# Kernel tuning notes

Measured on AMD Instinct MI355X. Metric: run time of the kernel, lower is better.

Reference implementation:

```python
import jax, jax.numpy as jnp
import numpy as np


def setup_inputs() -> dict:
    key = jax.random.key(0)
    ks = jax.random.split(key, 13)
    B, T, F = 4096, 512, 64
    P, M = 64, 64  # price / metrics embedding dims
    TD, ED = 1, 8  # target_dim, explanatory_dim
    s = 0.05
    return {
        "input_seq": jax.random.normal(ks[0], (B, T, F), jnp.float32),
        "m_Wih": jax.random.normal(ks[1], (M, F + P), jnp.float32) * s,
        "m_Whh": jax.random.normal(ks[2], (M, M), jnp.float32) * s,
        "m_bih": jax.random.normal(ks[3], (M,), jnp.float32) * s,
        "m_bhh": jax.random.normal(ks[4], (M,), jnp.float32) * s,
        "p_Wih": jax.random.normal(ks[5], (P, F + M), jnp.float32) * s,
        "p_Whh": jax.random.normal(ks[6], (P, P), jnp.float32) * s,
        "p_bih": jax.random.normal(ks[7], (P,), jnp.float32) * s,
        "p_bhh": jax.random.normal(ks[8], (P,), jnp.float32) * s,
        "price_lin_W": jax.random.normal(ks[9], (TD, P), jnp.float32) * s,
        "price_lin_b": jax.random.normal(ks[10], (TD,), jnp.float32) * s,
        "metrics_lin_W": jax.random.normal(ks[11], (ED, M), jnp.float32) * s,
        "metrics_lin_b": jax.random.normal(ks[12], (ED,), jnp.float32) * s,
    }


def reference(input_seq, m_Wih, m_Whh, m_bih, m_bhh,
              p_Wih, p_Whh, p_bih, p_bhh,
              price_lin_W, price_lin_b, metrics_lin_W, metrics_lin_b):
    B = input_seq.shape[0]
    P = p_Whh.shape[0]
    M = m_Whh.shape[0]
    p0 = jnp.zeros((B, P), input_seq.dtype)
    m0 = jnp.zeros((B, M), input_seq.dtype)

    def step(carry, x_t):  # x_t: [B, F]
        p, m = carry
        # metrics cell: input = cat(x_t, price_embedding)
        m = jnp.tanh(jnp.concatenate([x_t, p], axis=1) @ m_Wih.T + m_bih
                     + m @ m_Whh.T + m_bhh)
        # price cell: input = cat(x_t, metrics_embedding)
        p = jnp.tanh(jnp.concatenate([x_t, m], axis=1) @ p_Wih.T + p_bih
                     + p @ p_Whh.T + p_bhh)
        return (p, m), None

    (p, m), _ = jax.lax.scan(step, (p0, m0), jnp.swapaxes(input_seq, 0, 1))
    # dropout in eval mode = identity
    price_pred = p @ price_lin_W.T + price_lin_b
    metrics_pred = m @ metrics_lin_W.T + metrics_lin_b
    return (price_pred, metrics_pred)
```

## Files before the change

kernel.cpp:

```cpp
#include <hip/hip_runtime.h>

typedef short bf16x8 __attribute__((ext_vector_type(8)));
typedef float f32x4 __attribute__((ext_vector_type(4)));
typedef int   int4v  __attribute__((ext_vector_type(4)));

#define MFMA16(a, b, c) __builtin_amdgcn_mfma_f32_16x16x32_bf16((a), (b), (c), 0, 0, 0)

static constexpr int T_LEN = 512;
static constexpr int F_DIM = 64;
static constexpr int NB    = 8;
static constexpr float C1  = 2.885390081777927f;

__device__ __forceinline__ unsigned short brne(float f) {
  unsigned u = __float_as_uint(f);
  return (unsigned short)((u + 0x7fffu + ((u >> 16) & 1u)) >> 16);
}

__device__ __forceinline__ int cvtpk(float lo, float hi) {
  int r;
  asm("v_cvt_pk_bf16_f32 %0, %1, %2" : "=v"(r) : "v"(lo), "v"(hi));
  return r;
}

__device__ __forceinline__ bf16x8 cvt8(const float4 &a, const float4 &b) {
  int4v d = {cvtpk(a.x, a.y), cvtpk(a.z, a.w), cvtpk(b.x, b.y), cvtpk(b.z, b.w)};
  union { int4v i; bf16x8 h; } u;
  u.i = d;
  return u.h;
}

__device__ __forceinline__ void swap32(float &a, float &b) {
  auto r = __builtin_amdgcn_permlane32_swap(__float_as_int(a), __float_as_int(b),
                                            false, false);
  a = __int_as_float(r[0]);
  b = __int_as_float(r[1]);
}

__device__ __forceinline__ float xor1(float v) {
  return __int_as_float(__builtin_amdgcn_mov_dpp(__float_as_int(v), 0xB1, 0xF, 0xF, true));
}

__device__ __forceinline__ float tanh_fold(float s, float c2) {
  float e  = __builtin_amdgcn_exp2f(__builtin_fmaf(s, C1, c2));
  float rc = __builtin_amdgcn_rcpf(e + 1.0f);
  return __builtin_fmaf(-2.0f, rc, 1.0f);
}

__device__ __forceinline__ void bar() {
  asm volatile("s_waitcnt lgkmcnt(0)" ::: "memory");
  __builtin_amdgcn_s_barrier();
  __builtin_amdgcn_sched_barrier(0);
}

template<int PAR, bool FIN>
__device__ __forceinline__ void epilogue(
    const f32x4 &a0, const f32x4 &a1, float c2,
    unsigned short (*buf)[72], float (*fin)[68],
    int wofs, bool evn, int rowA, int j)
{
  float z0 = a0[0] + a1[0];
  float z1 = a0[1] + a1[1];
  float z2 = a0[2] + a1[2];
  float z3 = a0[3] + a1[3];
  swap32(z0, z2);
  swap32(z1, z3);
  float sA = (PAR == 0) ? z0 : z2;
  float sB = (PAR == 0) ? z1 : z3;
  float tA = tanh_fold(sA, c2);
  float tB = tanh_fold(sB, c2);
  float nA = xor1(tA);
  float nB = xor1(tB);
  if (evn) {
    unsigned short *p = &buf[0][0];
    *(unsigned *)(p + wofs)      = (unsigned)cvtpk(tA, nA);
    *(unsigned *)(p + wofs + 72) = (unsigned)cvtpk(tB, nB);
  }
  if (FIN) {
    fin[rowA][j]     = tA;
    fin[rowA + 1][j] = tB;
  }
}

template<int PAR, bool FIN>
__device__ __forceinline__ void step_cells(
    int arow, int g8, int j, int wofs, bool evn, int rowA,
    const bf16x8 &x0, const bf16x8 &x1,
    const bf16x8 (&Bm)[6], const bf16x8 (&Bp)[6],
    float c2m, float c2p, const f32x4 &Z,
    unsigned short (*sm_c)[72], unsigned short (*sm_p)[72],
    unsigned short (*sp_c)[72], unsigned short (*sp_p)[72],
    float (*mfin)[68], float (*pfin)[68])
{
  bf16x8 p0 = *(const bf16x8 *)&sp_p[arow][g8];
  bf16x8 p1 = *(const bf16x8 *)&sp_p[arow][32 + g8];
  bf16x8 m0 = *(const bf16x8 *)&sm_p[arow][g8];
  bf16x8 m1 = *(const bf16x8 *)&sm_p[arow][32 + g8];

  f32x4 a0 = MFMA16(x0, Bm[0], Z);
  f32x4 a1 = MFMA16(x1, Bm[1], Z);
  a0 = MFMA16(p0, Bm[2], a0);
  a1 = MFMA16(p1, Bm[3], a1);
  a0 = MFMA16(m0, Bm[4], a0);
  a1 = MFMA16(m1, Bm[5], a1);
  f32x4 b0 = MFMA16(x0, Bp[0], Z);
  f32x4 b1 = MFMA16(x1, Bp[1], Z);
  b0 = MFMA16(p0, Bp[4], b0);
  b1 = MFMA16(p1, Bp[5], b1);
  epilogue<PAR, FIN>(a0, a1, c2m, sm_c, mfin, wofs, evn, rowA, j);
  bar();
  {
    bf16x8 n0 = *(const bf16x8 *)&sm_c[arow][g8];
    bf16x8 n1 = *(const bf16x8 *)&sm_c[arow][32 + g8];
    b0 = MFMA16(n0, Bp[2], b0);
    b1 = MFMA16(n1, Bp[3], b1);
    epilogue<PAR, FIN>(b0, b1, c2p, sp_c, pfin, wofs, evn, rowA, j);
  }
  bar();
}

__global__ __launch_bounds__(256, 2)
void mr_rnn_kernel(const float *__restrict__ x,
                   const float *__restrict__ mWih, const float *__restrict__ mWhh,
                   const float *__restrict__ mbih, const float *__restrict__ mbhh,
                   const float *__restrict__ pWih, const float *__restrict__ pWhh,
                   const float *__restrict__ pbih, const float *__restrict__ pbhh,
                   const float *__restrict__ plW,  const float *__restrict__ plb,
                   const float *__restrict__ mlW,  const float *__restrict__ mlb,
                   float *__restrict__ out, int B)
{
  __shared__ __align__(16) unsigned short sm[2][NB][72], sp[2][NB][72];
  __shared__ __align__(16) float s_mfin[NB][68], s_pfin[NB][68];

  const int tid  = threadIdx.x;
  const int lane = tid & 63;
  const int q    = tid >> 6;
  const int l15  = lane & 15;
  const int arow = l15 & (NB - 1);
  const int half = l15 >> 3;
  const int g    = lane >> 4;
  const int j    = q * 16 + l15;
  const int b0   = blockIdx.x * NB;
  const int g8   = g * 8;
  const int rowA = ((lane & 16) >> 2) | ((lane >> 5) << 1);
  const bool evn = (l15 & 1) == 0;
  const int wofs = rowA * 72 + (j & ~1);

  bf16x8 Bm[6], Bp[6];
#pragma unroll
  for (int kt = 0; kt < 6; ++kt) {
    const int k0 = kt * 32 + g8;
#pragma unroll
    for (int i = 0; i < 8; ++i) {
      const int k = k0 + i;
      float wm = (k < 128) ? mWih[j * 128 + k] : mWhh[j * 64 + (k - 128)];
      float wp = (k < 128) ? pWih[j * 128 + k] : pWhh[j * 64 + (k - 128)];
      Bm[kt][i] = (short)brne(wm);
      Bp[kt][i] = (short)brne(wp);
    }
  }
  const float c2m = C1 * (mbih[j] + mbhh[j]);
  const float c2p = C1 * (pbih[j] + pbhh[j]);
  const f32x4 Z = {0.f, 0.f, 0.f, 0.f};

  for (int idx = tid; idx < NB * 72; idx += 256) {
    const int bb = idx / 72, kk = idx % 72;
    sm[1][bb][kk] = 0;
    sp[1][bb][kk] = 0;
  }

  const float *pxl = x + ((size_t)(b0 + arow) * T_LEN + half) * F_DIM + g8;
  float4 A0 = *(const float4 *)(pxl);
  float4 A1 = *(const float4 *)(pxl + 4);
  float4 A2 = *(const float4 *)(pxl + 32);
  float4 A3 = *(const float4 *)(pxl + 36);
  bf16x8 x0 = cvt8(A0, A1);
  bf16x8 x1 = cvt8(A2, A3);
  __syncthreads();

#pragma unroll 1
  for (int t = 0; t < T_LEN - 2; t += 2) {
    pxl += 2 * F_DIM;
    A0 = *(const float4 *)(pxl);
    A1 = *(const float4 *)(pxl + 4);
    A2 = *(const float4 *)(pxl + 32);
    A3 = *(const float4 *)(pxl + 36);
    step_cells<0, false>(arow, g8, j, wofs, evn, rowA, x0, x1, Bm, Bp, c2m, c2p, Z,
                         sm[0], sm[1], sp[0], sp[1], s_mfin, s_pfin);
    step_cells<1, false>(arow, g8, j, wofs, evn, rowA, x0, x1, Bm, Bp, c2m, c2p, Z,
                         sm[1], sm[0], sp[1], sp[0], s_mfin, s_pfin);
    x0 = cvt8(A0, A1);
    x1 = cvt8(A2, A3);
  }
  step_cells<0, false>(arow, g8, j, wofs, evn, rowA, x0, x1, Bm, Bp, c2m, c2p, Z,
                       sm[0], sm[1], sp[0], sp[1], s_mfin, s_pfin);
  step_cells<1, true>(arow, g8, j, wofs, evn, rowA, x0, x1, Bm, Bp, c2m, c2p, Z,
                      sm[1], sm[0], sp[1], sp[0], s_mfin, s_pfin);

  if (tid < NB) {
    const int b = tid;
    float acc = plb[0];
#pragma unroll 1
    for (int k = 0; k < 64; ++k) acc += s_pfin[b][k] * plW[k];
    out[b0 + b] = acc;
  } else if (tid < NB + NB * 8) {
    const int r = tid - NB;
    const int b = r >> 3, e = r & 7;
    float acc = mlb[e];
#pragma unroll 1
    for (int k = 0; k < 64; ++k) acc += s_mfin[b][k] * mlW[e * 64 + k];
    out[(size_t)B + (size_t)(b0 + b) * 8 + e] = acc;
  }
}

extern "C" void kernel_launch(void* const* d_in, const int* in_sizes, int n_in,
                              void* d_out, int out_size, void* d_ws, size_t ws_size,
                              hipStream_t stream) {
  (void)n_in; (void)out_size; (void)d_ws; (void)ws_size;
  const float* x    = (const float*)d_in[0];
  const float* mWih = (const float*)d_in[1];
  const float* mWhh = (const float*)d_in[2];
  const float* mbih = (const float*)d_in[3];
  const float* mbhh = (const float*)d_in[4];
  const float* pWih = (const float*)d_in[5];
  const float* pWhh = (const float*)d_in[6];
  const float* pbih = (const float*)d_in[7];
  const float* pbhh = (const float*)d_in[8];
  const float* plW  = (const float*)d_in[9];
  const float* plb  = (const float*)d_in[10];
  const float* mlW  = (const float*)d_in[11];
  const float* mlb  = (const float*)d_in[12];
  const int B = in_sizes[0] / (T_LEN * F_DIM);
  const int nblk = B / NB;
  mr_rnn_kernel<<<dim3(nblk), dim3(256), 0, stream>>>(
      x, mWih, mWhh, mbih, mbhh, pWih, pWhh, pbih, pbhh,
      plW, plb, mlW, mlb, (float*)d_out, B);
}
```

Before: 292.0 us.

## Keep metrics state in registers, reorder MFMAs, add setprio around compute

The previous metrics hidden state, which each lane already read back for the price cell, is now carried in registers instead of re-read from a double-buffered LDS array, so the metrics buffer becomes single-buffered. The price-cell x and p MFMAs move after the barrier instead of running before the metrics epilogue. s_setprio is raised around the MFMA/epilogue sections, and the custom barrier is replaced with __syncthreads. This shortens the critical path before the first barrier and cuts LDS reads, but puts more MFMA work after the barrier and relies on __syncthreads for correct LDS reuse ordering.

```diff
diff --git a/kernel.cpp b/kernel.cpp
--- a/kernel.cpp
+++ b/kernel.cpp
@@ -44,12 +44,6 @@
   float e  = __builtin_amdgcn_exp2f(__builtin_fmaf(s, C1, c2));
   float rc = __builtin_amdgcn_rcpf(e + 1.0f);
   return __builtin_fmaf(-2.0f, rc, 1.0f);
-}
-
-__device__ __forceinline__ void bar() {
-  asm volatile("s_waitcnt lgkmcnt(0)" ::: "memory");
-  __builtin_amdgcn_s_barrier();
-  __builtin_amdgcn_sched_barrier(0);
 }
 
 template<int PAR, bool FIN>
@@ -85,37 +79,44 @@
 __device__ __forceinline__ void step_cells(
     int arow, int g8, int j, int wofs, bool evn, int rowA,
     const bf16x8 &x0, const bf16x8 &x1,
+    bf16x8 &mo0, bf16x8 &mo1,
     const bf16x8 (&Bm)[6], const bf16x8 (&Bp)[6],
     float c2m, float c2p, const f32x4 &Z,
-    unsigned short (*sm_c)[72], unsigned short (*sm_p)[72],
+    unsigned short (*sm)[72],
     unsigned short (*sp_c)[72], unsigned short (*sp_p)[72],
     float (*mfin)[68], float (*pfin)[68])
 {
   bf16x8 p0 = *(const bf16x8 *)&sp_p[arow][g8];
   bf16x8 p1 = *(const bf16x8 *)&sp_p[arow][32 + g8];
-  bf16x8 m0 = *(const bf16x8 *)&sm_p[arow][g8];
-  bf16x8 m1 = *(const bf16x8 *)&sm_p[arow][32 + g8];
-
-  f32x4 a0 = MFMA16(x0, Bm[0], Z);
-  f32x4 a1 = MFMA16(x1, Bm[1], Z);
-  a0 = MFMA16(p0, Bm[2], a0);
-  a1 = MFMA16(p1, Bm[3], a1);
-  a0 = MFMA16(m0, Bm[4], a0);
-  a1 = MFMA16(m1, Bm[5], a1);
-  f32x4 b0 = MFMA16(x0, Bp[0], Z);
-  f32x4 b1 = MFMA16(x1, Bp[1], Z);
-  b0 = MFMA16(p0, Bp[4], b0);
-  b1 = MFMA16(p1, Bp[5], b1);
-  epilogue<PAR, FIN>(a0, a1, c2m, sm_c, mfin, wofs, evn, rowA, j);
-  bar();
+
+  __builtin_amdgcn_s_setprio(1);
   {
-    bf16x8 n0 = *(const bf16x8 *)&sm_c[arow][g8];
-    bf16x8 n1 = *(const bf16x8 *)&sm_c[arow][32 + g8];
+    f32x4 a0 = MFMA16(x0, Bm[0], Z);
+    f32x4 a1 = MFMA16(x1, Bm[1], Z);
+    a0 = MFMA16(p0, Bm[2], a0);
+    a1 = MFMA16(p1, Bm[3], a1);
+    a0 = MFMA16(mo0, Bm[4], a0);
+    a1 = MFMA16(mo1, Bm[5], a1);
+    epilogue<PAR, FIN>(a0, a1, c2m, sm, mfin, wofs, evn, rowA, j);
+  }
+  __builtin_amdgcn_s_setprio(0);
+  __syncthreads();
+  {
+    bf16x8 n0 = *(const bf16x8 *)&sm[arow][g8];
+    bf16x8 n1 = *(const bf16x8 *)&sm[arow][32 + g8];
+    __builtin_amdgcn_s_setprio(1);
+    f32x4 b0 = MFMA16(x0, Bp[0], Z);
+    f32x4 b1 = MFMA16(x1, Bp[1], Z);
     b0 = MFMA16(n0, Bp[2], b0);
     b1 = MFMA16(n1, Bp[3], b1);
+    b0 = MFMA16(p0, Bp[4], b0);
+    b1 = MFMA16(p1, Bp[5], b1);
     epilogue<PAR, FIN>(b0, b1, c2p, sp_c, pfin, wofs, evn, rowA, j);
-  }
-  bar();
+    __builtin_amdgcn_s_setprio(0);
+    mo0 = n0;
+    mo1 = n1;
+  }
+  __syncthreads();
 }
 
 __global__ __launch_bounds__(256, 2)
@@ -128,7 +129,8 @@
                    const float *__restrict__ mlW,  const float *__restrict__ mlb,
                    float *__restrict__ out, int B)
 {
-  __shared__ __align__(16) unsigned short sm[2][NB][72], sp[2][NB][72];
+  __shared__ __align__(16) unsigned short sm[NB][72];
+  __shared__ __align__(16) unsigned short sp[2][NB][72];
   __shared__ __align__(16) float s_mfin[NB][68], s_pfin[NB][68];
 
   const int tid  = threadIdx.x;
@@ -164,9 +166,10 @@
 
   for (int idx = tid; idx < NB * 72; idx += 256) {
     const int bb = idx / 72, kk = idx % 72;
-    sm[1][bb][kk] = 0;
     sp[1][bb][kk] = 0;
   }
+  bf16x8 mo0 = {0, 0, 0, 0, 0, 0, 0, 0};
+  bf16x8 mo1 = {0, 0, 0, 0, 0, 0, 0, 0};
 
   const float *pxl = x + ((size_t)(b0 + arow) * T_LEN + half) * F_DIM + g8;
   float4 A0 = *(const float4 *)(pxl);
@@ -184,17 +187,21 @@
     A1 = *(const float4 *)(pxl + 4);
     A2 = *(const float4 *)(pxl + 32);
     A3 = *(const float4 *)(pxl + 36);
-    step_cells<0, false>(arow, g8, j, wofs, evn, rowA, x0, x1, Bm, Bp, c2m, c2p, Z,
-                         sm[0], sm[1], sp[0], sp[1], s_mfin, s_pfin);
-    step_cells<1, false>(arow, g8, j, wofs, evn, rowA, x0, x1, Bm, Bp, c2m, c2p, Z,
-                         sm[1], sm[0], sp[1], sp[0], s_mfin, s_pfin);
+    step_cells<0, false>(arow, g8, j, wofs, evn, rowA, x0, x1, mo0, mo1,
+                         Bm, Bp, c2m, c2p, Z,
+                         sm, sp[0], sp[1], s_mfin, s_pfin);
+    step_cells<1, false>(arow, g8, j, wofs, evn, rowA, x0, x1, mo0, mo1,
+                         Bm, Bp, c2m, c2p, Z,
+                         sm, sp[1], sp[0], s_mfin, s_pfin);
     x0 = cvt8(A0, A1);
     x1 = cvt8(A2, A3);
   }
-  step_cells<0, false>(arow, g8, j, wofs, evn, rowA, x0, x1, Bm, Bp, c2m, c2p, Z,
-                       sm[0], sm[1], sp[0], sp[1], s_mfin, s_pfin);
-  step_cells<1, true>(arow, g8, j, wofs, evn, rowA, x0, x1, Bm, Bp, c2m, c2p, Z,
-                      sm[1], sm[0], sp[1], sp[0], s_mfin, s_pfin);
+  step_cells<0, false>(arow, g8, j, wofs, evn, rowA, x0, x1, mo0, mo1,
+                       Bm, Bp, c2m, c2p, Z,
+                       sm, sp[0], sp[1], s_mfin, s_pfin);
+  step_cells<1, true>(arow, g8, j, wofs, evn, rowA, x0, x1, mo0, mo1,
+                      Bm, Bp, c2m, c2p, Z,
+                      sm, sp[1], sp[0], s_mfin, s_pfin);
 
   if (tid < NB) {
     const int b = tid;
```

Result: faster. 270.3 us (-7.4%).
